# Kernel optimization log

Measured on AMD Instinct MI355X. Metric: run time of the kernel, lower is better.

## Reference

```python
import jax, jax.numpy as jnp
import numpy as np

DIM = 768
HEADS = 12
HEAD_DIM = DIM // HEADS
EPS = 1e-5


def setup_inputs() -> dict:
    key = jax.random.key(0)
    ks = jax.random.split(key, 9)
    s = 0.02
    x = jax.random.normal(ks[0], (4, 1024, DIM), dtype=jnp.float32)
    return {
        "x": x,
        "Wqkv_c": jax.random.normal(ks[1], (DIM, 3 * DIM), jnp.float32) * s,
        "bqkv_c": jnp.zeros((3 * DIM,), jnp.float32),
        "Wp_c": jax.random.normal(ks[2], (DIM, DIM), jnp.float32) * s,
        "bp_c": jnp.zeros((DIM,), jnp.float32),
        "Wqkv_ac": jax.random.normal(ks[3], (DIM, 3 * DIM), jnp.float32) * s,
        "bqkv_ac": jnp.zeros((3 * DIM,), jnp.float32),
        "Wp_ac": jax.random.normal(ks[4], (DIM, DIM), jnp.float32) * s,
        "bp_ac": jnp.zeros((DIM,), jnp.float32),
        "gamma": jnp.ones((DIM,), jnp.float32),
        "beta": jnp.zeros((DIM,), jnp.float32),
    }


def _branch(x, Wqkv, bqkv, Wp, bp, causal: bool):
    B, T, C = x.shape
    qkv = (x @ Wqkv + bqkv).reshape(B, T, 3, HEADS, HEAD_DIM)
    qkv = jnp.transpose(qkv, (2, 0, 3, 1, 4))  # [3,B,H,T,Dh]
    q, k, v = qkv[0], qkv[1], qkv[2]
    scores = jnp.einsum("bhqd,bhkd->bhqk", q, k) / np.sqrt(HEAD_DIM).astype(np.float32)
    i = jnp.arange(T)[:, None]
    j = jnp.arange(T)[None, :]
    mask = (j <= i) if causal else (j >= i)  # tril / triu (incl. diagonal)
    scores = jnp.where(mask[None, None], scores, -jnp.inf)
    attn = jax.nn.softmax(scores, axis=-1)
    out = jnp.einsum("bhqk,bhkd->bhqd", attn, v)
    out = jnp.transpose(out, (0, 2, 1, 3)).reshape(B, T, C)
    return out @ Wp + bp


def reference(x, Wqkv_c, bqkv_c, Wp_c, bp_c, Wqkv_ac, bqkv_ac, Wp_ac, bp_ac, gamma, beta):
    out_c = _branch(x, Wqkv_c, bqkv_c, Wp_c, bp_c, causal=True)
    out_ac = _branch(x, Wqkv_ac, bqkv_ac, Wp_ac, bp_ac, causal=False)
    y = x + out_c + out_ac  # residual; dropout is identity at eval
    mu = jnp.mean(y, axis=-1, keepdims=True)
    var = jnp.var(y, axis=-1, keepdims=True)
    return (y - mu) * jax.lax.rsqrt(var + EPS) * gamma + beta
```

## Files before the change

kernel.cpp:

```cpp
#include <hip/hip_runtime.h>
#include <stdint.h>

#define DIM 768
#define HEADS 12
#define HD 64
#define BATCH 4
#define SEQ 1024
#define NTOK (BATCH*SEQ)
#define QKVW (3*DIM)
#define QKW (2*DIM)
#define EPS 1e-5f

typedef __attribute__((ext_vector_type(8))) short short8;
typedef __attribute__((ext_vector_type(4))) float f32x4;

__device__ __forceinline__ unsigned short f2bf(float f) {
    union { float f; unsigned u; } v; v.f = f;
    unsigned r = v.u + 0x7fffu + ((v.u >> 16) & 1u);
    return (unsigned short)(r >> 16);
}
__device__ __forceinline__ float b2f(unsigned short s) {
    union { unsigned u; float f; } v; v.u = (unsigned)s << 16; return v.f;
}

__device__ __forceinline__ void gld_lds16(const void* g, void* l) {
    auto gp = reinterpret_cast<const __attribute__((address_space(1))) unsigned int*>(
        (uintptr_t)g);
    auto lp = reinterpret_cast<__attribute__((address_space(3))) unsigned int*>(
        (unsigned int)(uintptr_t)l);
    __builtin_amdgcn_global_load_lds(gp, lp, 16, 0, 0);
}

#define CVT_X_BLOCKS (NTOK*DIM/4096)
#define CVT_WQ_TILES ((QKVW/32)*(DIM/32))
#define CVT_WP_TILES ((DIM/32)*(DIM/32))
__global__ __launch_bounds__(256) void cvt_all_kernel(
    const float* __restrict__ x,
    const float* __restrict__ Wq0, const float* __restrict__ Wq1,
    const float* __restrict__ Wp0, const float* __restrict__ Wp1,
    unsigned short* __restrict__ xb,
    unsigned short* __restrict__ WqT0, unsigned short* __restrict__ WqT1,
    unsigned short* __restrict__ WpT0, unsigned short* __restrict__ WpT1)
{
    const int bid = blockIdx.x, tid = threadIdx.x;
    if (bid < CVT_X_BLOCKS) {
        const int base = bid * 1024 + tid;
#pragma unroll
        for (int u = 0; u < 4; ++u) {
            const float4 v = ((const float4*)x)[base + u * 256];
            ushort4 o4;
            o4.x = f2bf(v.x); o4.y = f2bf(v.y); o4.z = f2bf(v.z); o4.w = f2bf(v.w);
            ((ushort4*)xb)[base + u * 256] = o4;
        }
        return;
    }
    __shared__ float t[32][33];
    const float* W; unsigned short* WT; int N, K, tile;
    int w = bid - CVT_X_BLOCKS;
    if (w < 2 * CVT_WQ_TILES) {
        const int z = w / CVT_WQ_TILES; tile = w % CVT_WQ_TILES;
        W = z ? Wq1 : Wq0; WT = z ? WqT1 : WqT0; N = QKVW; K = DIM;
    } else {
        w -= 2 * CVT_WQ_TILES;
        const int z = w / CVT_WP_TILES; tile = w % CVT_WP_TILES;
        W = z ? Wp1 : Wp0; WT = z ? WpT1 : WpT0; N = DIM; K = DIM;
    }
    const int ntiles = N / 32;
    const int n0 = (tile % ntiles) * 32, k0 = (tile / ntiles) * 32;
    const int c = tid & 31, rr = tid >> 5;
#pragma unroll
    for (int i = 0; i < 4; ++i)
        t[rr + 8 * i][c] = W[(size_t)(k0 + rr + 8 * i) * N + n0 + c];
    __syncthreads();
#pragma unroll
    for (int i = 0; i < 4; ++i)
        WT[(size_t)(n0 + rr + 8 * i) * K + k0 + c] = f2bf(t[c][rr + 8 * i]);
}

__global__ __launch_bounds__(256, 2) void gemm_qkv_kernel(
    const unsigned short* __restrict__ A,
    const unsigned short* __restrict__ BT0, const unsigned short* __restrict__ BT1,
    const float* __restrict__ bias0, const float* __restrict__ bias1,
    unsigned short* __restrict__ QK0, unsigned short* __restrict__ QK1,
    unsigned short* __restrict__ VT0, unsigned short* __restrict__ VT1)
{
    const int gid = blockIdx.x;
    const int wg = (gid & 7) * 144 + (gid >> 3);
    const int by = wg & 31;
    const int bxz = wg >> 5;
    const int z = (bxz >= 18) ? 1 : 0;
    const int bx = z ? bxz - 18 : bxz;
    const unsigned short* __restrict__ BT = z ? BT1 : BT0;
    const float* __restrict__ bias = z ? bias1 : bias0;
    unsigned short* __restrict__ QK = z ? QK1 : QK0;
    unsigned short* __restrict__ VT = z ? VT1 : VT0;
    const int m0 = by * 128;
    const int nb0 = bx * 128;

    __shared__ __align__(16) unsigned short lds[32768];

    const int tid = threadIdx.x, lane = tid & 63, wv = tid >> 6;
    const int fm = lane & 15, fg = lane >> 4;
    const int wr = wv >> 1, wc = wv & 1;

    const int sr8 = lane >> 3;
    const int sc = ((lane & 7) ^ sr8) * 8;
    const unsigned short* pA = A  + (size_t)(m0  + wv * 8 + sr8) * DIM + sc;
    const unsigned short* pB = BT + (size_t)(nb0 + wv * 8 + sr8) * DIM + sc;
    unsigned short* dA = lds + wv * 512;
    unsigned short* dB = lds + 16384 + wv * 512;

    const int swz = fm & 7;
    const int cK0 = ((0 + fg) ^ swz) * 8;
    const int cK1 = ((4 + fg) ^ swz) * 8;
    const int aB = (wr * 64 + fm) * 64;
    const int bB = (wc * 64 + fm) * 64;

    f32x4 acc[4][4];
#pragma unroll
    for (int i = 0; i < 4; ++i)
#pragma unroll
        for (int j = 0; j < 4; ++j) acc[i][j] = f32x4{0.f, 0.f, 0.f, 0.f};

    short8 a[4][2], b[4][2];

#pragma unroll
    for (int j = 0; j < 4; ++j) {
        gld_lds16(pA + j * 32 * DIM, dA + j * 2048);
        gld_lds16(pB + j * 32 * DIM, dB + j * 2048);
    }

    for (int t = 0; t < 12; ++t) {
        const int ab = (t & 1) * 8192;
        const int bb = 16384 + (t & 1) * 8192;
        const int nb2 = ((t + 1) & 1) * 8192;

        asm volatile("s_waitcnt vmcnt(0)" ::: "memory");
        __builtin_amdgcn_s_barrier();
        if (t < 11) {
            const int kN = (t + 1) * 64;
#pragma unroll
            for (int j = 0; j < 4; ++j) {
                gld_lds16(pA + kN + j * 32 * DIM, dA + nb2 + j * 2048);
                gld_lds16(pB + kN + j * 32 * DIM, dB + nb2 + j * 2048);
            }
        }

#pragma unroll
        for (int mi = 0; mi < 4; ++mi) {
            a[mi][0] = *(const short8*)&lds[ab + aB + mi * 1024 + cK0];
            a[mi][1] = *(const short8*)&lds[ab + aB + mi * 1024 + cK1];
        }
#pragma unroll
        for (int nj = 0; nj < 2; ++nj) {
            b[nj][0] = *(const short8*)&lds[bb + bB + nj * 1024 + cK0];
            b[nj][1] = *(const short8*)&lds[bb + bB + nj * 1024 + cK1];
        }
        asm volatile("s_waitcnt lgkmcnt(0)" ::: "memory");
        __builtin_amdgcn_sched_barrier(0);
        __builtin_amdgcn_s_setprio(1);
#pragma unroll
        for (int ks = 0; ks < 2; ++ks)
#pragma unroll
            for (int mi = 0; mi < 4; ++mi)
#pragma unroll
                for (int nj = 0; nj < 2; ++nj)
                    acc[mi][nj] = __builtin_amdgcn_mfma_f32_16x16x32_bf16(
                        a[mi][ks], b[nj][ks], acc[mi][nj], 0, 0, 0);
        __builtin_amdgcn_s_setprio(0);

#pragma unroll
        for (int nj = 2; nj < 4; ++nj) {
            b[nj][0] = *(const short8*)&lds[bb + bB + nj * 1024 + cK0];
            b[nj][1] = *(const short8*)&lds[bb + bB + nj * 1024 + cK1];
        }
        asm volatile("s_waitcnt lgkmcnt(0)" ::: "memory");
        __builtin_amdgcn_sched_barrier(0);
        __builtin_amdgcn_s_setprio(1);
#pragma unroll
        for (int ks = 0; ks < 2; ++ks)
#pragma unroll
            for (int mi = 0; mi < 4; ++mi)
#pragma unroll
                for (int nj = 2; nj < 4; ++nj)
                    acc[mi][nj] = __builtin_amdgcn_mfma_f32_16x16x32_bf16(
                        a[mi][ks], b[nj][ks], acc[mi][nj], 0, 0, 0);
        __builtin_amdgcn_s_setprio(0);
    }

    __syncthreads();
    const int rbase = fg * 4;
    const int rowg = tid >> 4, lseg = tid & 15;
    if (nb0 < QKW) {
        const float qsc = (nb0 < DIM) ? 0.125f : 1.0f;
#pragma unroll
        for (int i = 0; i < 4; ++i) {
            const int ml = wr * 64 + i * 16 + rbase;
#pragma unroll
            for (int j = 0; j < 4; ++j) {
                const int nl = wc * 64 + j * 16 + fm;
                const float bs = bias[nb0 + nl];
#pragma unroll
                for (int r = 0; r < 4; ++r)
                    lds[(ml + r) * 136 + nl] = f2bf((acc[i][j][r] + bs) * qsc);
            }
        }
        __syncthreads();
#pragma unroll
        for (int pp = 0; pp < 8; ++pp) {
            const int row = pp * 16 + rowg;
            const uint4 v = *(const uint4*)&lds[row * 136 + lseg * 8];
            *(uint4*)(QK + (size_t)(m0 + row) * QKW + nb0 + lseg * 8) = v;
        }
    } else {
        const int b8 = m0 >> 10, t0 = m0 & 1023;
#pragma unroll
        for (int i = 0; i < 4; ++i) {
            const int tl = wr * 64 + i * 16 + rbase;
#pragma unroll
            for (int j = 0; j < 4; ++j) {
                const int nl = wc * 64 + j * 16 + fm;
                const float bs = bias[nb0 + nl];
                const unsigned p0 = f2bf(acc[i][j][0] + bs);
                const unsigned p1 = f2bf(acc[i][j][1] + bs);
                const unsigned p2 = f2bf(acc[i][j][2] + bs);
                const unsigned p3 = f2bf(acc[i][j][3] + bs);
                uint2 u; u.x = p0 | (p1 << 16); u.y = p2 | (p3 << 16);
                *(uint2*)(&lds[nl * 136 + tl]) = u;
            }
        }
        __syncthreads();
#pragma unroll
        for (int pp = 0; pp < 8; ++pp) {
            const int nl = pp * 16 + rowg;
            const int nh = (nb0 - QKW) + nl;
            const uint4 v = *(const uint4*)&lds[nl * 136 + lseg * 8];
            *(uint4*)(VT + ((size_t)((b8 * HEADS + (nh >> 6)) * HD + (nh & 63))) * SEQ
                      + t0 + lseg * 8) = v;
        }
    }
}

__global__ __launch_bounds__(256) void gemm_proj_kernel(
    const unsigned short* __restrict__ A0, const unsigned short* __restrict__ BT0,
    const unsigned short* __restrict__ A1, const unsigned short* __restrict__ BT1,
    const float* __restrict__ b0, const float* __restrict__ b1,
    const float* __restrict__ xres, float* __restrict__ Y0,
    unsigned short* __restrict__ Y1)
{
    const int z = blockIdx.z;
    const unsigned short* __restrict__ A  = z ? A1 : A0;
    const unsigned short* __restrict__ BT = z ? BT1 : BT0;
    __shared__ __align__(16) unsigned short Als[2][64 * 32];
    __shared__ __align__(16) unsigned short Bls[2][128 * 32];
    const int tid = threadIdx.x, lane = tid & 63, wv = tid >> 6;
    const int m0 = blockIdx.y * 64, n0 = blockIdx.x * 128;
    const int fm = lane & 15, fg = lane >> 4, fk = (lane >> 4) * 8;
    const int srw = lane >> 2, kk = (lane & 3) * 8;
    const int K = DIM;

    const unsigned short* Ag  = A  + (size_t)(m0 + wv * 16 + srw) * K + kk;
    const unsigned short* Bg0 = BT + (size_t)(n0 + wv * 32 + srw) * K + kk;
    const unsigned short* Bg1 = BT + (size_t)(n0 + wv * 32 + 16 + srw) * K + kk;

    f32x4 acc[4][2];
#pragma unroll
    for (int i = 0; i < 4; ++i)
#pragma unroll
        for (int j = 0; j < 2; ++j) acc[i][j] = f32x4{0.f, 0.f, 0.f, 0.f};

    gld_lds16(Ag,  &Als[0][wv * 512]);
    gld_lds16(Bg0, &Bls[0][wv * 1024]);
    gld_lds16(Bg1, &Bls[0][wv * 1024 + 512]);

    const int NK = K / 32;
    for (int kt = 0; kt < NK; ++kt) {
        const int p = kt & 1;
        __syncthreads();
        if (kt + 1 < NK) {
            const int off = (kt + 1) * 32;
            gld_lds16(Ag + off,  &Als[p ^ 1][wv * 512]);
            gld_lds16(Bg0 + off, &Bls[p ^ 1][wv * 1024]);
            gld_lds16(Bg1 + off, &Bls[p ^ 1][wv * 1024 + 512]);
        }
        short8 af[4], bf[2];
#pragma unroll
        for (int i = 0; i < 4; ++i)
            af[i] = *(const short8*)&Als[p][(i * 16 + fm) * 32 + fk];
#pragma unroll
        for (int j = 0; j < 2; ++j)
            bf[j] = *(const short8*)&Bls[p][(wv * 32 + j * 16 + fm) * 32 + fk];
#pragma unroll
        for (int i = 0; i < 4; ++i)
#pragma unroll
            for (int j = 0; j < 2; ++j)
                acc[i][j] = __builtin_amdgcn_mfma_f32_16x16x32_bf16(af[i], bf[j], acc[i][j], 0, 0, 0);
    }
#pragma unroll
    for (int i = 0; i < 4; ++i) {
        const int m = m0 + i * 16 + fg * 4;
#pragma unroll
        for (int j = 0; j < 2; ++j) {
            const int n = n0 + wv * 32 + j * 16 + fm;
            if (z == 0) {
                const float bs = b0[n] + b1[n];
#pragma unroll
                for (int r = 0; r < 4; ++r) {
                    const size_t idx = (size_t)(m + r) * DIM + n;
                    Y0[idx] = acc[i][j][r] + xres[idx] + bs;
                }
            } else {
#pragma unroll
                for (int r = 0; r < 4; ++r)
                    Y1[(size_t)(m + r) * DIM + n] = f2bf(acc[i][j][r]);
            }
        }
    }
}

#define KP 72
__global__ __launch_bounds__(256, 3) void attn_fused_kernel(
    const unsigned short* __restrict__ qk_c, const unsigned short* __restrict__ vT_c,
    const unsigned short* __restrict__ qk_ac, const unsigned short* __restrict__ vT_ac,
    unsigned short* __restrict__ o_c, unsigned short* __restrict__ o_ac)
{
    __shared__ __align__(16) unsigned short Kls[2][64 * KP];
    __shared__ __align__(16) unsigned short Vls[2][64 * KP];
    __shared__ __align__(16) unsigned short Ps[4][16 * KP];
    const int tid = threadIdx.x, lane = tid & 63, w = tid >> 6;
    const int fm = lane & 15, fg = lane >> 4;
    const int bh = blockIdx.x, qt = blockIdx.y;
    const int b = bh / HEADS, h = bh % HEADS;
    unsigned short* Psw = &Ps[w][0];
    const int srow = tid >> 3, sseg = (tid & 7) * 8;

    for (int br = 0; br < 2; ++br) {
        const int causal = (br == 0);
        const unsigned short* __restrict__ qk = causal ? qk_c : qk_ac;
        const unsigned short* __restrict__ vT = causal ? vT_c : vT_ac;
        unsigned short* __restrict__ o = causal ? o_c : o_ac;
        const unsigned short* qbase = qk + (size_t)b * SEQ * QKW + h * HD;
        const unsigned short* kbase = qbase + DIM;
        const unsigned short* vtb   = vT + (size_t)(b * HEADS + h) * HD * SEQ;

        short8 qb0, qb1;
        {
            const size_t qoff = (size_t)(qt * 64 + w * 16 + fm) * QKW + fg * 8;
            qb0 = *(const short8*)(qbase + qoff);
            qb1 = *(const short8*)(qbase + qoff + 32);
        }

        float ls = 0.f;
        f32x4 accO[4];
#pragma unroll
        for (int dj = 0; dj < 4; ++dj) accO[dj] = f32x4{0.f, 0.f, 0.f, 0.f};

        const int ktb = causal ? 0 : qt;
        const int kte = causal ? qt : (SEQ / 64 - 1);

        uint4 kr0 = *(const uint4*)(kbase + (size_t)(ktb * 64 + srow) * QKW + sseg);
        uint4 kr1 = *(const uint4*)(kbase + (size_t)(ktb * 64 + srow + 32) * QKW + sseg);
        uint4 vr0 = *(const uint4*)(vtb + (size_t)srow * SEQ + ktb * 64 + sseg);
        uint4 vr1 = *(const uint4*)(vtb + (size_t)(srow + 32) * SEQ + ktb * 64 + sseg);

        if (br) __syncthreads();
        int p = 0;
        for (int kt = ktb; kt <= kte; ++kt) {
            *(uint4*)(&Kls[p][srow * KP + sseg])        = kr0;
            *(uint4*)(&Kls[p][(srow + 32) * KP + sseg]) = kr1;
            *(uint4*)(&Vls[p][srow * KP + sseg])        = vr0;
            *(uint4*)(&Vls[p][(srow + 32) * KP + sseg]) = vr1;
            if (kt < kte) {
                const int ktn = kt + 1;
                kr0 = *(const uint4*)(kbase + (size_t)(ktn * 64 + srow) * QKW + sseg);
                kr1 = *(const uint4*)(kbase + (size_t)(ktn * 64 + srow + 32) * QKW + sseg);
                vr0 = *(const uint4*)(vtb + (size_t)srow * SEQ + ktn * 64 + sseg);
                vr1 = *(const uint4*)(vtb + (size_t)(srow + 32) * SEQ + ktn * 64 + sseg);
            }
            __syncthreads();

            f32x4 st[4];
#pragma unroll
            for (int kj = 0; kj < 4; ++kj) {
                const short8 ka0 = *(const short8*)&Kls[p][(kj * 16 + fm) * KP + fg * 8];
                const short8 ka1 = *(const short8*)&Kls[p][(kj * 16 + fm) * KP + 32 + fg * 8];
                st[kj] = __builtin_amdgcn_mfma_f32_16x16x32_bf16(ka0, qb0, f32x4{0.f,0.f,0.f,0.f}, 0, 0, 0);
                st[kj] = __builtin_amdgcn_mfma_f32_16x16x32_bf16(ka1, qb1, st[kj], 0, 0, 0);
            }
            const bool diag = (kt == qt);
#pragma unroll
            for (int kj = 0; kj < 4; ++kj) {
                float e[4];
#pragma unroll
                for (int r = 0; r < 4; ++r) {
                    float v = st[kj][r];
                    if (diag) {
                        const int ki = kj * 16 + fg * 4 + r;
                        const int qi = w * 16 + fm;
                        const bool ok = causal ? (ki <= qi) : (ki >= qi);
                        if (!ok) v = -1e30f;
                    }
                    e[r] = __expf(v);
                    ls += e[r];
                }
                union { float f; unsigned u; } u0, u1, u2, u3;
                u0.f = e[0]; u1.f = e[1]; u2.f = e[2]; u3.f = e[3];
                uint2 u;
                u.x = (u0.u >> 16) | (u1.u & 0xffff0000u);
                u.y = (u2.u >> 16) | (u3.u & 0xffff0000u);
                *(uint2*)(Psw + fm * KP + kj * 16 + fg * 4) = u;
            }
            const short8 ap0 = *(const short8*)(Psw + fm * KP + fg * 8);
            const short8 ap1 = *(const short8*)(Psw + fm * KP + 32 + fg * 8);
#pragma unroll
            for (int dj = 0; dj < 4; ++dj) {
                const short8 vb0 = *(const short8*)&Vls[p][(dj * 16 + fm) * KP + fg * 8];
                const short8 vb1 = *(const short8*)&Vls[p][(dj * 16 + fm) * KP + 32 + fg * 8];
                accO[dj] = __builtin_amdgcn_mfma_f32_16x16x32_bf16(ap0, vb0, accO[dj], 0, 0, 0);
                accO[dj] = __builtin_amdgcn_mfma_f32_16x16x32_bf16(ap1, vb1, accO[dj], 0, 0, 0);
            }
            p ^= 1;
        }

        float lt = ls;
        lt += __shfl_xor(lt, 16);
        lt += __shfl_xor(lt, 32);
        float li_o[4];
#pragma unroll
        for (int r = 0; r < 4; ++r) li_o[r] = __shfl(lt, fg * 4 + r);
#pragma unroll
        for (int r = 0; r < 4; ++r) {
            const float inv = 1.f / li_o[r];
            const int q = qt * 64 + w * 16 + fg * 4 + r;
            unsigned short* orow = o + ((size_t)b * SEQ + q) * DIM + h * HD;
#pragma unroll
            for (int dj = 0; dj < 4; ++dj)
                orow[dj * 16 + fm] = f2bf(accO[dj][r] * inv);
        }
    }
}

__global__ __launch_bounds__(256) void ln_kernel(
    const float* __restrict__ Y0, const unsigned short* __restrict__ Y1,
    const float* __restrict__ gamma, const float* __restrict__ beta,
    float* __restrict__ out)
{
    const int row = blockIdx.x;
    const int tid = threadIdx.x;
    const float* y0r = Y0 + (size_t)row * DIM;
    const unsigned short* y1r = Y1 + (size_t)row * DIM;
    float v0 = y0r[tid]       + b2f(y1r[tid]);
    float v1 = y0r[tid + 256] + b2f(y1r[tid + 256]);
    float v2 = y0r[tid + 512] + b2f(y1r[tid + 512]);
    float s = v0 + v1 + v2;
    float q = v0 * v0 + v1 * v1 + v2 * v2;
#pragma unroll
    for (int off = 32; off > 0; off >>= 1) {
        s += __shfl_down(s, off);
        q += __shfl_down(q, off);
    }
    __shared__ float rs_[4], rq_[4];
    const int wv = tid >> 6;
    if ((tid & 63) == 0) { rs_[wv] = s; rq_[wv] = q; }
    __syncthreads();
    const float ts = rs_[0] + rs_[1] + rs_[2] + rs_[3];
    const float tq = rq_[0] + rq_[1] + rq_[2] + rq_[3];
    const float mu = ts * (1.f / DIM);
    const float var = tq * (1.f / DIM) - mu * mu;
    const float rstd = rsqrtf(var + EPS);
    out[(size_t)row * DIM + tid]       = (v0 - mu) * rstd * gamma[tid]       + beta[tid];
    out[(size_t)row * DIM + tid + 256] = (v1 - mu) * rstd * gamma[tid + 256] + beta[tid + 256];
    out[(size_t)row * DIM + tid + 512] = (v2 - mu) * rstd * gamma[tid + 512] + beta[tid + 512];
}

extern "C" void kernel_launch(void* const* d_in, const int* in_sizes, int n_in,
                              void* d_out, int out_size, void* d_ws, size_t ws_size,
                              hipStream_t stream)
{
    const float* x       = (const float*)d_in[0];
    const float* Wqkv_c  = (const float*)d_in[1];
    const float* bqkv_c  = (const float*)d_in[2];
    const float* Wp_c    = (const float*)d_in[3];
    const float* bp_c    = (const float*)d_in[4];
    const float* Wqkv_ac = (const float*)d_in[5];
    const float* bqkv_ac = (const float*)d_in[6];
    const float* Wp_ac   = (const float*)d_in[7];
    const float* bp_ac   = (const float*)d_in[8];
    const float* gamma   = (const float*)d_in[9];
    const float* beta    = (const float*)d_in[10];
    float* out = (float*)d_out;

    char* p = (char*)d_ws;
    unsigned short* qk_c   = (unsigned short*)p; p += (size_t)NTOK * QKW * 2;
    unsigned short* qk_ac  = (unsigned short*)p; p += (size_t)NTOK * QKW * 2;
    unsigned short* vT_c   = (unsigned short*)p; p += (size_t)NTOK * DIM * 2;
    unsigned short* vT_ac  = (unsigned short*)p; p += (size_t)NTOK * DIM * 2;
    unsigned short* o_ac   = (unsigned short*)p; p += (size_t)NTOK * DIM * 2;
    unsigned short* xb     = (unsigned short*)p; p += (size_t)NTOK * DIM * 2;
    unsigned short* WqT_c  = (unsigned short*)p; p += (size_t)QKVW * DIM * 2;
    unsigned short* WqT_ac = (unsigned short*)p; p += (size_t)QKVW * DIM * 2;
    unsigned short* WpT_c  = (unsigned short*)p; p += (size_t)DIM * DIM * 2;
    unsigned short* WpT_ac = (unsigned short*)p; p += (size_t)DIM * DIM * 2;
    unsigned short* o_c = WqT_c;
    float*          Y0  = (float*)qk_c;
    unsigned short* Y1  = vT_c;

    cvt_all_kernel<<<CVT_X_BLOCKS + 2 * CVT_WQ_TILES + 2 * CVT_WP_TILES, 256, 0, stream>>>(
        x, Wqkv_c, Wqkv_ac, Wp_c, Wp_ac, xb, WqT_c, WqT_ac, WpT_c, WpT_ac);

    gemm_qkv_kernel<<<1152, 256, 0, stream>>>(
        xb, WqT_c, WqT_ac, bqkv_c, bqkv_ac, qk_c, qk_ac, vT_c, vT_ac);

    attn_fused_kernel<<<dim3(BATCH * HEADS, SEQ / 64), 256, 0, stream>>>(
        qk_c, vT_c, qk_ac, vT_ac, o_c, o_ac);

    gemm_proj_kernel<<<dim3(DIM / 128, NTOK / 64, 2), 256, 0, stream>>>(
        o_c, WpT_c, o_ac, WpT_ac, bp_c, bp_ac, x, Y0, Y1);
    ln_kernel<<<NTOK, 256, 0, stream>>>(Y0, Y1, gamma, beta, out);
}
```

Baseline: 197.1 us.

## Share A tile across both branch weight matrices in QKV GEMM with triple buffering

Each workgroup of the QKV GEMM now computes the same 128x128 output tile for both the causal and anticausal weights, loading the activation tile once and reusing it across two accumulator sets. That halves the grid and the A-operand global and LDS traffic. The K loop also moves from a double-buffered 64-wide step to a triple-buffered 32-wide step with a partial vmcnt wait, so loads run two stages ahead. The cost is twice the accumulator registers and a larger LDS footprint, which may lower occupancy, plus fewer workgroups to fill the GPU.

```diff
diff --git a/kernel.cpp b/kernel.cpp
--- a/kernel.cpp
+++ b/kernel.cpp
@@ -85,148 +85,140 @@
     unsigned short* __restrict__ VT0, unsigned short* __restrict__ VT1)
 {
     const int gid = blockIdx.x;
-    const int wg = (gid & 7) * 144 + (gid >> 3);
-    const int by = wg & 31;
-    const int bxz = wg >> 5;
-    const int z = (bxz >= 18) ? 1 : 0;
-    const int bx = z ? bxz - 18 : bxz;
-    const unsigned short* __restrict__ BT = z ? BT1 : BT0;
-    const float* __restrict__ bias = z ? bias1 : bias0;
-    unsigned short* __restrict__ QK = z ? QK1 : QK0;
-    unsigned short* __restrict__ VT = z ? VT1 : VT0;
+    const int wg = (gid & 7) * 72 + (gid >> 3);
+    const int by = wg & 31, bx = wg >> 5;
     const int m0 = by * 128;
     const int nb0 = bx * 128;
 
-    __shared__ __align__(16) unsigned short lds[32768];
+    __shared__ __align__(16) unsigned short lds[36864];
 
     const int tid = threadIdx.x, lane = tid & 63, wv = tid >> 6;
     const int fm = lane & 15, fg = lane >> 4;
     const int wr = wv >> 1, wc = wv & 1;
 
-    const int sr8 = lane >> 3;
-    const int sc = ((lane & 7) ^ sr8) * 8;
-    const unsigned short* pA = A  + (size_t)(m0  + wv * 8 + sr8) * DIM + sc;
-    const unsigned short* pB = BT + (size_t)(nb0 + wv * 8 + sr8) * DIM + sc;
-    unsigned short* dA = lds + wv * 512;
-    unsigned short* dB = lds + 16384 + wv * 512;
-
-    const int swz = fm & 7;
-    const int cK0 = ((0 + fg) ^ swz) * 8;
-    const int cK1 = ((4 + fg) ^ swz) * 8;
-    const int aB = (wr * 64 + fm) * 64;
-    const int bB = (wc * 64 + fm) * 64;
-
-    f32x4 acc[4][4];
+    const int s4 = lane >> 2;
+    const int sc = ((lane & 3) ^ ((lane >> 3) & 3)) * 8;
+    const unsigned short* pA  = A   + (size_t)(m0  + wv * 16 + s4) * DIM + sc;
+    const unsigned short* pBc = BT0 + (size_t)(nb0 + wv * 16 + s4) * DIM + sc;
+    const unsigned short* pBa = BT1 + (size_t)(nb0 + wv * 16 + s4) * DIM + sc;
+    unsigned short* dA  = lds + wv * 512;
+    unsigned short* dBc = lds + 12288 + wv * 512;
+    unsigned short* dBa = lds + 24576 + wv * 512;
+
+    const int cR = (fg ^ ((fm >> 1) & 3)) * 8;
+    const int aB = (wr * 64 + fm) * 32;
+    const int bB = (wc * 64 + fm) * 32;
+
+    f32x4 accc[4][4], acca[4][4];
 #pragma unroll
     for (int i = 0; i < 4; ++i)
 #pragma unroll
-        for (int j = 0; j < 4; ++j) acc[i][j] = f32x4{0.f, 0.f, 0.f, 0.f};
-
-    short8 a[4][2], b[4][2];
-
-#pragma unroll
-    for (int j = 0; j < 4; ++j) {
-        gld_lds16(pA + j * 32 * DIM, dA + j * 2048);
-        gld_lds16(pB + j * 32 * DIM, dB + j * 2048);
-    }
-
-    for (int t = 0; t < 12; ++t) {
-        const int ab = (t & 1) * 8192;
-        const int bb = 16384 + (t & 1) * 8192;
-        const int nb2 = ((t + 1) & 1) * 8192;
-
-        asm volatile("s_waitcnt vmcnt(0)" ::: "memory");
+        for (int j = 0; j < 4; ++j) {
+            accc[i][j] = f32x4{0.f, 0.f, 0.f, 0.f};
+            acca[i][j] = f32x4{0.f, 0.f, 0.f, 0.f};
+        }
+
+    short8 a[4], b[4], b2[4];
+
+#define STAGE(kt, buf) do {                                   \
+        const int ko_ = (kt) * 32; const int bo_ = (buf) * 4096; \
+        gld_lds16(pA  + ko_,            dA  + bo_);           \
+        gld_lds16(pA  + ko_ + 64 * DIM, dA  + bo_ + 2048);    \
+        gld_lds16(pBc + ko_,            dBc + bo_);           \
+        gld_lds16(pBc + ko_ + 64 * DIM, dBc + bo_ + 2048);    \
+        gld_lds16(pBa + ko_,            dBa + bo_);           \
+        gld_lds16(pBa + ko_ + 64 * DIM, dBa + bo_ + 2048);    \
+    } while (0)
+
+    STAGE(0, 0);
+    STAGE(1, 1);
+
+#pragma unroll 3
+    for (int t = 0; t < 24; ++t) {
+        if (t < 23) asm volatile("s_waitcnt vmcnt(6)" ::: "memory");
+        else        asm volatile("s_waitcnt vmcnt(0)" ::: "memory");
         __builtin_amdgcn_s_barrier();
-        if (t < 11) {
-            const int kN = (t + 1) * 64;
-#pragma unroll
-            for (int j = 0; j < 4; ++j) {
-                gld_lds16(pA + kN + j * 32 * DIM, dA + nb2 + j * 2048);
-                gld_lds16(pB + kN + j * 32 * DIM, dB + nb2 + j * 2048);
-            }
-        }
-
-#pragma unroll
-        for (int mi = 0; mi < 4; ++mi) {
-            a[mi][0] = *(const short8*)&lds[ab + aB + mi * 1024 + cK0];
-            a[mi][1] = *(const short8*)&lds[ab + aB + mi * 1024 + cK1];
-        }
-#pragma unroll
-        for (int nj = 0; nj < 2; ++nj) {
-            b[nj][0] = *(const short8*)&lds[bb + bB + nj * 1024 + cK0];
-            b[nj][1] = *(const short8*)&lds[bb + bB + nj * 1024 + cK1];
-        }
+        if (t < 22) STAGE(t + 2, (t + 2) % 3);
+        const int ab = (t % 3) * 4096;
+
+#pragma unroll
+        for (int mi = 0; mi < 4; ++mi)
+            a[mi] = *(const short8*)&lds[ab + aB + mi * 512 + cR];
+#pragma unroll
+        for (int nj = 0; nj < 4; ++nj)
+            b[nj] = *(const short8*)&lds[12288 + ab + bB + nj * 512 + cR];
         asm volatile("s_waitcnt lgkmcnt(0)" ::: "memory");
         __builtin_amdgcn_sched_barrier(0);
         __builtin_amdgcn_s_setprio(1);
 #pragma unroll
-        for (int ks = 0; ks < 2; ++ks)
-#pragma unroll
-            for (int mi = 0; mi < 4; ++mi)
-#pragma unroll
-                for (int nj = 0; nj < 2; ++nj)
-                    acc[mi][nj] = __builtin_amdgcn_mfma_f32_16x16x32_bf16(
-                        a[mi][ks], b[nj][ks], acc[mi][nj], 0, 0, 0);
+        for (int mi = 0; mi < 4; ++mi)
+#pragma unroll
+            for (int nj = 0; nj < 4; ++nj)
+                accc[mi][nj] = __builtin_amdgcn_mfma_f32_16x16x32_bf16(
+                    a[mi], b[nj], accc[mi][nj], 0, 0, 0);
         __builtin_amdgcn_s_setprio(0);
 
 #pragma unroll
-        for (int nj = 2; nj < 4; ++nj) {
-            b[nj][0] = *(const short8*)&lds[bb + bB + nj * 1024 + cK0];
-            b[nj][1] = *(const short8*)&lds[bb + bB + nj * 1024 + cK1];
-        }
+        for (int nj = 0; nj < 4; ++nj)
+            b2[nj] = *(const short8*)&lds[24576 + ab + bB + nj * 512 + cR];
         asm volatile("s_waitcnt lgkmcnt(0)" ::: "memory");
         __builtin_amdgcn_sched_barrier(0);
         __builtin_amdgcn_s_setprio(1);
 #pragma unroll
-        for (int ks = 0; ks < 2; ++ks)
-#pragma unroll
-            for (int mi = 0; mi < 4; ++mi)
-#pragma unroll
-                for (int nj = 2; nj < 4; ++nj)
-                    acc[mi][nj] = __builtin_amdgcn_mfma_f32_16x16x32_bf16(
-                        a[mi][ks], b[nj][ks], acc[mi][nj], 0, 0, 0);
+        for (int mi = 0; mi < 4; ++mi)
+#pragma unroll
+            for (int nj = 0; nj < 4; ++nj)
+                acca[mi][nj] = __builtin_amdgcn_mfma_f32_16x16x32_bf16(
+                    a[mi], b2[nj], acca[mi][nj], 0, 0, 0);
         __builtin_amdgcn_s_setprio(0);
     }
+#undef STAGE
 
     __syncthreads();
-    const int rbase = fg * 4;
     const int rowg = tid >> 4, lseg = tid & 15;
     if (nb0 < QKW) {
         const float qsc = (nb0 < DIM) ? 0.125f : 1.0f;
 #pragma unroll
         for (int i = 0; i < 4; ++i) {
-            const int ml = wr * 64 + i * 16 + rbase;
+            const int ml = wr * 64 + i * 16 + fg * 4;
 #pragma unroll
             for (int j = 0; j < 4; ++j) {
                 const int nl = wc * 64 + j * 16 + fm;
-                const float bs = bias[nb0 + nl];
-#pragma unroll
-                for (int r = 0; r < 4; ++r)
-                    lds[(ml + r) * 136 + nl] = f2bf((acc[i][j][r] + bs) * qsc);
+                const float bsc = bias0[nb0 + nl];
+                const float bsa = bias1[nb0 + nl];
+#pragma unroll
+                for (int r = 0; r < 4; ++r) {
+                    lds[(ml + r) * 136 + nl]         = f2bf((accc[i][j][r] + bsc) * qsc);
+                    lds[17408 + (ml + r) * 136 + nl] = f2bf((acca[i][j][r] + bsa) * qsc);
+                }
             }
         }
         __syncthreads();
 #pragma unroll
         for (int pp = 0; pp < 8; ++pp) {
             const int row = pp * 16 + rowg;
-            const uint4 v = *(const uint4*)&lds[row * 136 + lseg * 8];
-            *(uint4*)(QK + (size_t)(m0 + row) * QKW + nb0 + lseg * 8) = v;
+            const uint4 vc = *(const uint4*)&lds[row * 136 + lseg * 8];
+            const uint4 va = *(const uint4*)&lds[17408 + row * 136 + lseg * 8];
+            *(uint4*)(QK0 + (size_t)(m0 + row) * QKW + nb0 + lseg * 8) = vc;
+            *(uint4*)(QK1 + (size_t)(m0 + row) * QKW + nb0 + lseg * 8) = va;
         }
     } else {
         const int b8 = m0 >> 10, t0 = m0 & 1023;
 #pragma unroll
         for (int i = 0; i < 4; ++i) {
-            const int tl = wr * 64 + i * 16 + rbase;
+            const int tl = wr * 64 + i * 16 + fg * 4;
 #pragma unroll
             for (int j = 0; j < 4; ++j) {
                 const int nl = wc * 64 + j * 16 + fm;
-                const float bs = bias[nb0 + nl];
-                const unsigned p0 = f2bf(acc[i][j][0] + bs);
-                const unsigned p1 = f2bf(acc[i][j][1] + bs);
-                const unsigned p2 = f2bf(acc[i][j][2] + bs);
-                const unsigned p3 = f2bf(acc[i][j][3] + bs);
-                uint2 u; u.x = p0 | (p1 << 16); u.y = p2 | (p3 << 16);
-                *(uint2*)(&lds[nl * 136 + tl]) = u;
+                const float bsc = bias0[nb0 + nl];
+                const float bsa = bias1[nb0 + nl];
+                uint2 uc, ua;
+                uc.x = (unsigned)f2bf(accc[i][j][0] + bsc) | ((unsigned)f2bf(accc[i][j][1] + bsc) << 16);
+                uc.y = (unsigned)f2bf(accc[i][j][2] + bsc) | ((unsigned)f2bf(accc[i][j][3] + bsc) << 16);
+                ua.x = (unsigned)f2bf(acca[i][j][0] + bsa) | ((unsigned)f2bf(acca[i][j][1] + bsa) << 16);
+                ua.y = (unsigned)f2bf(acca[i][j][2] + bsa) | ((unsigned)f2bf(acca[i][j][3] + bsa) << 16);
+                *(uint2*)(&lds[nl * 136 + tl])         = uc;
+                *(uint2*)(&lds[17408 + nl * 136 + tl]) = ua;
             }
         }
         __syncthreads();
@@ -234,9 +226,12 @@
         for (int pp = 0; pp < 8; ++pp) {
             const int nl = pp * 16 + rowg;
             const int nh = (nb0 - QKW) + nl;
-            const uint4 v = *(const uint4*)&lds[nl * 136 + lseg * 8];
-            *(uint4*)(VT + ((size_t)((b8 * HEADS + (nh >> 6)) * HD + (nh & 63))) * SEQ
-                      + t0 + lseg * 8) = v;
+            const size_t voff = ((size_t)((b8 * HEADS + (nh >> 6)) * HD + (nh & 63))) * SEQ
+                                + t0 + lseg * 8;
+            const uint4 vc = *(const uint4*)&lds[nl * 136 + lseg * 8];
+            const uint4 va = *(const uint4*)&lds[17408 + nl * 136 + lseg * 8];
+            *(uint4*)(VT0 + voff) = vc;
+            *(uint4*)(VT1 + voff) = va;
         }
     }
 }
@@ -508,7 +503,7 @@
     cvt_all_kernel<<<CVT_X_BLOCKS + 2 * CVT_WQ_TILES + 2 * CVT_WP_TILES, 256, 0, stream>>>(
         x, Wqkv_c, Wqkv_ac, Wp_c, Wp_ac, xb, WqT_c, WqT_ac, WpT_c, WpT_ac);
 
-    gemm_qkv_kernel<<<1152, 256, 0, stream>>>(
+    gemm_qkv_kernel<<<576, 256, 0, stream>>>(
         xb, WqT_c, WqT_ac, bqkv_c, bqkv_ac, qk_c, qk_ac, vT_c, vT_ac);
 
     attn_fused_kernel<<<dim3(BATCH * HEADS, SEQ / 64), 256, 0, stream>>>(
```

After: 195.8 us. Within noise of the previous version (-0.6%).

## Halve QKV GEMM K-tile to cut LDS and raise occupancy to four blocks

Applied to the files above, without the earlier changes.

The QKV GEMM now stages K in 32-wide slices instead of 64-wide, shrinking the double-buffered LDS footprint from 64KB to about 34KB. Launch bounds are raised to allow 4 blocks per CU, and the swizzle and block-to-tile mapping are reworked into a 2x4 grouping for L2 locality. The aim is more resident waves to hide global-load latency. The cost is twice as many barrier and wait iterations per tile and tighter register limits, which could cause spills.

```diff
diff --git a/kernel.cpp b/kernel.cpp
--- a/kernel.cpp
+++ b/kernel.cpp
@@ -77,7 +77,7 @@
         WT[(size_t)(n0 + rr + 8 * i) * K + k0 + c] = f2bf(t[c][rr + 8 * i]);
 }
 
-__global__ __launch_bounds__(256, 2) void gemm_qkv_kernel(
+__global__ __launch_bounds__(256, 4) void gemm_qkv_kernel(
     const unsigned short* __restrict__ A,
     const unsigned short* __restrict__ BT0, const unsigned short* __restrict__ BT1,
     const float* __restrict__ bias0, const float* __restrict__ bias1,
@@ -85,9 +85,9 @@
     unsigned short* __restrict__ VT0, unsigned short* __restrict__ VT1)
 {
     const int gid = blockIdx.x;
-    const int wg = (gid & 7) * 144 + (gid >> 3);
-    const int by = wg & 31;
-    const int bxz = wg >> 5;
+    const int g = gid & 7, l = gid >> 3;
+    const int by  = (g >> 2) * 16 + (l & 15);
+    const int bxz = (g & 3) * 9 + (l >> 4);
     const int z = (bxz >= 18) ? 1 : 0;
     const int bx = z ? bxz - 18 : bxz;
     const unsigned short* __restrict__ BT = z ? BT1 : BT0;
@@ -97,24 +97,22 @@
     const int m0 = by * 128;
     const int nb0 = bx * 128;
 
-    __shared__ __align__(16) unsigned short lds[32768];
+    __shared__ __align__(16) unsigned short lds[17408];
 
     const int tid = threadIdx.x, lane = tid & 63, wv = tid >> 6;
     const int fm = lane & 15, fg = lane >> 4;
     const int wr = wv >> 1, wc = wv & 1;
 
-    const int sr8 = lane >> 3;
-    const int sc = ((lane & 7) ^ sr8) * 8;
-    const unsigned short* pA = A  + (size_t)(m0  + wv * 8 + sr8) * DIM + sc;
-    const unsigned short* pB = BT + (size_t)(nb0 + wv * 8 + sr8) * DIM + sc;
+    const int s4 = lane >> 2;
+    const int sc = ((lane & 3) ^ ((lane >> 3) & 3)) * 8;
+    const unsigned short* pA = A  + (size_t)(m0  + wv * 16 + s4) * DIM + sc;
+    const unsigned short* pB = BT + (size_t)(nb0 + wv * 16 + s4) * DIM + sc;
     unsigned short* dA = lds + wv * 512;
-    unsigned short* dB = lds + 16384 + wv * 512;
-
-    const int swz = fm & 7;
-    const int cK0 = ((0 + fg) ^ swz) * 8;
-    const int cK1 = ((4 + fg) ^ swz) * 8;
-    const int aB = (wr * 64 + fm) * 64;
-    const int bB = (wc * 64 + fm) * 64;
+    unsigned short* dB = lds + 8192 + wv * 512;
+
+    const int cR = (fg ^ ((fm >> 1) & 3)) * 8;
+    const int aB = (wr * 64 + fm) * 32;
+    const int bB = (wc * 64 + fm) * 32;
 
     f32x4 acc[4][4];
 #pragma unroll
@@ -122,80 +120,64 @@
 #pragma unroll
         for (int j = 0; j < 4; ++j) acc[i][j] = f32x4{0.f, 0.f, 0.f, 0.f};
 
-    short8 a[4][2], b[4][2];
-
-#pragma unroll
-    for (int j = 0; j < 4; ++j) {
-        gld_lds16(pA + j * 32 * DIM, dA + j * 2048);
-        gld_lds16(pB + j * 32 * DIM, dB + j * 2048);
-    }
-
-    for (int t = 0; t < 12; ++t) {
-        const int ab = (t & 1) * 8192;
-        const int bb = 16384 + (t & 1) * 8192;
-        const int nb2 = ((t + 1) & 1) * 8192;
-
+    short8 a[4], b[4];
+
+#define STAGE(kt, buf) do {                                   \
+        const int ko_ = (kt) * 32; const int bo_ = (buf) * 4096; \
+        gld_lds16(pA + ko_,            dA + bo_);             \
+        gld_lds16(pA + ko_ + 64 * DIM, dA + bo_ + 2048);      \
+        gld_lds16(pB + ko_,            dB + bo_);             \
+        gld_lds16(pB + ko_ + 64 * DIM, dB + bo_ + 2048);      \
+    } while (0)
+
+    STAGE(0, 0);
+
+    for (int t = 0; t < 24; ++t) {
         asm volatile("s_waitcnt vmcnt(0)" ::: "memory");
         __builtin_amdgcn_s_barrier();
-        if (t < 11) {
-            const int kN = (t + 1) * 64;
-#pragma unroll
-            for (int j = 0; j < 4; ++j) {
-                gld_lds16(pA + kN + j * 32 * DIM, dA + nb2 + j * 2048);
-                gld_lds16(pB + kN + j * 32 * DIM, dB + nb2 + j * 2048);
-            }
-        }
-
-#pragma unroll
-        for (int mi = 0; mi < 4; ++mi) {
-            a[mi][0] = *(const short8*)&lds[ab + aB + mi * 1024 + cK0];
-            a[mi][1] = *(const short8*)&lds[ab + aB + mi * 1024 + cK1];
-        }
-#pragma unroll
-        for (int nj = 0; nj < 2; ++nj) {
-            b[nj][0] = *(const short8*)&lds[bb + bB + nj * 1024 + cK0];
-            b[nj][1] = *(const short8*)&lds[bb + bB + nj * 1024 + cK1];
-        }
+        if (t < 23) STAGE(t + 1, (t + 1) & 1);
+        const int ab = (t & 1) * 4096;
+
+#pragma unroll
+        for (int mi = 0; mi < 4; ++mi)
+            a[mi] = *(const short8*)&lds[ab + aB + mi * 512 + cR];
+#pragma unroll
+        for (int nj = 0; nj < 2; ++nj)
+            b[nj] = *(const short8*)&lds[8192 + ab + bB + nj * 512 + cR];
         asm volatile("s_waitcnt lgkmcnt(0)" ::: "memory");
         __builtin_amdgcn_sched_barrier(0);
         __builtin_amdgcn_s_setprio(1);
 #pragma unroll
-        for (int ks = 0; ks < 2; ++ks)
-#pragma unroll
-            for (int mi = 0; mi < 4; ++mi)
-#pragma unroll
-                for (int nj = 0; nj < 2; ++nj)
-                    acc[mi][nj] = __builtin_amdgcn_mfma_f32_16x16x32_bf16(
-                        a[mi][ks], b[nj][ks], acc[mi][nj], 0, 0, 0);
+        for (int mi = 0; mi < 4; ++mi)
+#pragma unroll
+            for (int nj = 0; nj < 2; ++nj)
+                acc[mi][nj] = __builtin_amdgcn_mfma_f32_16x16x32_bf16(
+                    a[mi], b[nj], acc[mi][nj], 0, 0, 0);
         __builtin_amdgcn_s_setprio(0);
 
 #pragma unroll
-        for (int nj = 2; nj < 4; ++nj) {
-            b[nj][0] = *(const short8*)&lds[bb + bB + nj * 1024 + cK0];
-            b[nj][1] = *(const short8*)&lds[bb + bB + nj * 1024 + cK1];
-        }
+        for (int nj = 2; nj < 4; ++nj)
+            b[nj] = *(const short8*)&lds[8192 + ab + bB + nj * 512 + cR];
         asm volatile("s_waitcnt lgkmcnt(0)" ::: "memory");
         __builtin_amdgcn_sched_barrier(0);
         __builtin_amdgcn_s_setprio(1);
 #pragma unroll
-        for (int ks = 0; ks < 2; ++ks)
-#pragma unroll
-            for (int mi = 0; mi < 4; ++mi)
-#pragma unroll
-                for (int nj = 2; nj < 4; ++nj)
-                    acc[mi][nj] = __builtin_amdgcn_mfma_f32_16x16x32_bf16(
-                        a[mi][ks], b[nj][ks], acc[mi][nj], 0, 0, 0);
+        for (int mi = 0; mi < 4; ++mi)
+#pragma unroll
+            for (int nj = 2; nj < 4; ++nj)
+                acc[mi][nj] = __builtin_amdgcn_mfma_f32_16x16x32_bf16(
+                    a[mi], b[nj], acc[mi][nj], 0, 0, 0);
         __builtin_amdgcn_s_setprio(0);
     }
+#undef STAGE
 
     __syncthreads();
-    const int rbase = fg * 4;
     const int rowg = tid >> 4, lseg = tid & 15;
     if (nb0 < QKW) {
         const float qsc = (nb0 < DIM) ? 0.125f : 1.0f;
 #pragma unroll
         for (int i = 0; i < 4; ++i) {
-            const int ml = wr * 64 + i * 16 + rbase;
+            const int ml = wr * 64 + i * 16 + fg * 4;
 #pragma unroll
             for (int j = 0; j < 4; ++j) {
                 const int nl = wc * 64 + j * 16 + fm;
@@ -216,16 +198,14 @@
         const int b8 = m0 >> 10, t0 = m0 & 1023;
 #pragma unroll
         for (int i = 0; i < 4; ++i) {
-            const int tl = wr * 64 + i * 16 + rbase;
+            const int tl = wr * 64 + i * 16 + fg * 4;
 #pragma unroll
             for (int j = 0; j < 4; ++j) {
                 const int nl = wc * 64 + j * 16 + fm;
                 const float bs = bias[nb0 + nl];
-                const unsigned p0 = f2bf(acc[i][j][0] + bs);
-                const unsigned p1 = f2bf(acc[i][j][1] + bs);
-                const unsigned p2 = f2bf(acc[i][j][2] + bs);
-                const unsigned p3 = f2bf(acc[i][j][3] + bs);
-                uint2 u; u.x = p0 | (p1 << 16); u.y = p2 | (p3 << 16);
+                uint2 u;
+                u.x = (unsigned)f2bf(acc[i][j][0] + bs) | ((unsigned)f2bf(acc[i][j][1] + bs) << 16);
+                u.y = (unsigned)f2bf(acc[i][j][2] + bs) | ((unsigned)f2bf(acc[i][j][3] + bs) << 16);
                 *(uint2*)(&lds[nl * 136 + tl]) = u;
             }
         }
```

Measured after the change: 195.1 us. About the same (-1.0%).

## Fuse both projection branches into one block and remap QKV GEMM tile order

Applied to the files above, without the earlier changes.

The projection GEMM now computes both the causal and anti-causal branches in the same block, with two accumulator sets, and writes a single fp32 sum plus residual and bias. This removes the bf16 intermediate Y1, its separate write and read, and the extra add in the layernorm kernel, and it halves the proj grid. The QKV GEMM block-to-tile mapping is also changed to group tiles differently across XCDs for L2 locality. The cost is doubled LDS and register use per proj block, which may lower occupancy, and fewer blocks in the proj launch.

```diff
diff --git a/kernel.cpp b/kernel.cpp
--- a/kernel.cpp
+++ b/kernel.cpp
@@ -85,9 +85,9 @@
     unsigned short* __restrict__ VT0, unsigned short* __restrict__ VT1)
 {
     const int gid = blockIdx.x;
-    const int wg = (gid & 7) * 144 + (gid >> 3);
-    const int by = wg & 31;
-    const int bxz = wg >> 5;
+    const int g = gid & 7, l = gid >> 3;
+    const int by  = (g >> 2) * 16 + (l & 15);
+    const int bxz = (g & 3) * 9 + (l >> 4);
     const int z = (bxz >= 18) ? 1 : 0;
     const int bx = z ? bxz - 18 : bxz;
     const unsigned short* __restrict__ BT = z ? BT1 : BT0;
@@ -189,13 +189,12 @@
     }
 
     __syncthreads();
-    const int rbase = fg * 4;
     const int rowg = tid >> 4, lseg = tid & 15;
     if (nb0 < QKW) {
         const float qsc = (nb0 < DIM) ? 0.125f : 1.0f;
 #pragma unroll
         for (int i = 0; i < 4; ++i) {
-            const int ml = wr * 64 + i * 16 + rbase;
+            const int ml = wr * 64 + i * 16 + fg * 4;
 #pragma unroll
             for (int j = 0; j < 4; ++j) {
                 const int nl = wc * 64 + j * 16 + fm;
@@ -216,16 +215,14 @@
         const int b8 = m0 >> 10, t0 = m0 & 1023;
 #pragma unroll
         for (int i = 0; i < 4; ++i) {
-            const int tl = wr * 64 + i * 16 + rbase;
+            const int tl = wr * 64 + i * 16 + fg * 4;
 #pragma unroll
             for (int j = 0; j < 4; ++j) {
                 const int nl = wc * 64 + j * 16 + fm;
                 const float bs = bias[nb0 + nl];
-                const unsigned p0 = f2bf(acc[i][j][0] + bs);
-                const unsigned p1 = f2bf(acc[i][j][1] + bs);
-                const unsigned p2 = f2bf(acc[i][j][2] + bs);
-                const unsigned p3 = f2bf(acc[i][j][3] + bs);
-                uint2 u; u.x = p0 | (p1 << 16); u.y = p2 | (p3 << 16);
+                uint2 u;
+                u.x = (unsigned)f2bf(acc[i][j][0] + bs) | ((unsigned)f2bf(acc[i][j][1] + bs) << 16);
+                u.y = (unsigned)f2bf(acc[i][j][2] + bs) | ((unsigned)f2bf(acc[i][j][3] + bs) << 16);
                 *(uint2*)(&lds[nl * 136 + tl]) = u;
             }
         }
@@ -245,33 +242,38 @@
     const unsigned short* __restrict__ A0, const unsigned short* __restrict__ BT0,
     const unsigned short* __restrict__ A1, const unsigned short* __restrict__ BT1,
     const float* __restrict__ b0, const float* __restrict__ b1,
-    const float* __restrict__ xres, float* __restrict__ Y0,
-    unsigned short* __restrict__ Y1)
+    const float* __restrict__ xres, float* __restrict__ Y)
 {
-    const int z = blockIdx.z;
-    const unsigned short* __restrict__ A  = z ? A1 : A0;
-    const unsigned short* __restrict__ BT = z ? BT1 : BT0;
-    __shared__ __align__(16) unsigned short Als[2][64 * 32];
-    __shared__ __align__(16) unsigned short Bls[2][128 * 32];
+    __shared__ __align__(16) unsigned short Als[2][2][64 * 32];
+    __shared__ __align__(16) unsigned short Bls[2][2][128 * 32];
     const int tid = threadIdx.x, lane = tid & 63, wv = tid >> 6;
     const int m0 = blockIdx.y * 64, n0 = blockIdx.x * 128;
     const int fm = lane & 15, fg = lane >> 4, fk = (lane >> 4) * 8;
     const int srw = lane >> 2, kk = (lane & 3) * 8;
     const int K = DIM;
 
-    const unsigned short* Ag  = A  + (size_t)(m0 + wv * 16 + srw) * K + kk;
-    const unsigned short* Bg0 = BT + (size_t)(n0 + wv * 32 + srw) * K + kk;
-    const unsigned short* Bg1 = BT + (size_t)(n0 + wv * 32 + 16 + srw) * K + kk;
-
-    f32x4 acc[4][2];
+    const unsigned short* Ag0  = A0  + (size_t)(m0 + wv * 16 + srw) * K + kk;
+    const unsigned short* Ag1  = A1  + (size_t)(m0 + wv * 16 + srw) * K + kk;
+    const unsigned short* Bg00 = BT0 + (size_t)(n0 + wv * 32 + srw) * K + kk;
+    const unsigned short* Bg01 = BT0 + (size_t)(n0 + wv * 32 + 16 + srw) * K + kk;
+    const unsigned short* Bg10 = BT1 + (size_t)(n0 + wv * 32 + srw) * K + kk;
+    const unsigned short* Bg11 = BT1 + (size_t)(n0 + wv * 32 + 16 + srw) * K + kk;
+
+    f32x4 acc0[4][2], acc1[4][2];
 #pragma unroll
     for (int i = 0; i < 4; ++i)
 #pragma unroll
-        for (int j = 0; j < 2; ++j) acc[i][j] = f32x4{0.f, 0.f, 0.f, 0.f};
-
-    gld_lds16(Ag,  &Als[0][wv * 512]);
-    gld_lds16(Bg0, &Bls[0][wv * 1024]);
-    gld_lds16(Bg1, &Bls[0][wv * 1024 + 512]);
+        for (int j = 0; j < 2; ++j) {
+            acc0[i][j] = f32x4{0.f, 0.f, 0.f, 0.f};
+            acc1[i][j] = f32x4{0.f, 0.f, 0.f, 0.f};
+        }
+
+    gld_lds16(Ag0,  &Als[0][0][wv * 512]);
+    gld_lds16(Bg00, &Bls[0][0][wv * 1024]);
+    gld_lds16(Bg01, &Bls[0][0][wv * 1024 + 512]);
+    gld_lds16(Ag1,  &Als[1][0][wv * 512]);
+    gld_lds16(Bg10, &Bls[1][0][wv * 1024]);
+    gld_lds16(Bg11, &Bls[1][0][wv * 1024 + 512]);
 
     const int NK = K / 32;
     for (int kt = 0; kt < NK; ++kt) {
@@ -279,22 +281,36 @@
         __syncthreads();
         if (kt + 1 < NK) {
             const int off = (kt + 1) * 32;
-            gld_lds16(Ag + off,  &Als[p ^ 1][wv * 512]);
-            gld_lds16(Bg0 + off, &Bls[p ^ 1][wv * 1024]);
-            gld_lds16(Bg1 + off, &Bls[p ^ 1][wv * 1024 + 512]);
+            gld_lds16(Ag0 + off,  &Als[0][p ^ 1][wv * 512]);
+            gld_lds16(Bg00 + off, &Bls[0][p ^ 1][wv * 1024]);
+            gld_lds16(Bg01 + off, &Bls[0][p ^ 1][wv * 1024 + 512]);
+            gld_lds16(Ag1 + off,  &Als[1][p ^ 1][wv * 512]);
+            gld_lds16(Bg10 + off, &Bls[1][p ^ 1][wv * 1024]);
+            gld_lds16(Bg11 + off, &Bls[1][p ^ 1][wv * 1024 + 512]);
         }
         short8 af[4], bf[2];
 #pragma unroll
         for (int i = 0; i < 4; ++i)
-            af[i] = *(const short8*)&Als[p][(i * 16 + fm) * 32 + fk];
+            af[i] = *(const short8*)&Als[0][p][(i * 16 + fm) * 32 + fk];
 #pragma unroll
         for (int j = 0; j < 2; ++j)
-            bf[j] = *(const short8*)&Bls[p][(wv * 32 + j * 16 + fm) * 32 + fk];
+            bf[j] = *(const short8*)&Bls[0][p][(wv * 32 + j * 16 + fm) * 32 + fk];
 #pragma unroll
         for (int i = 0; i < 4; ++i)
 #pragma unroll
             for (int j = 0; j < 2; ++j)
-                acc[i][j] = __builtin_amdgcn_mfma_f32_16x16x32_bf16(af[i], bf[j], acc[i][j], 0, 0, 0);
+                acc0[i][j] = __builtin_amdgcn_mfma_f32_16x16x32_bf16(af[i], bf[j], acc0[i][j], 0, 0, 0);
+#pragma unroll
+        for (int i = 0; i < 4; ++i)
+            af[i] = *(const short8*)&Als[1][p][(i * 16 + fm) * 32 + fk];
+#pragma unroll
+        for (int j = 0; j < 2; ++j)
+            bf[j] = *(const short8*)&Bls[1][p][(wv * 32 + j * 16 + fm) * 32 + fk];
+#pragma unroll
+        for (int i = 0; i < 4; ++i)
+#pragma unroll
+            for (int j = 0; j < 2; ++j)
+                acc1[i][j] = __builtin_amdgcn_mfma_f32_16x16x32_bf16(af[i], bf[j], acc1[i][j], 0, 0, 0);
     }
 #pragma unroll
     for (int i = 0; i < 4; ++i) {
@@ -302,17 +318,11 @@
 #pragma unroll
         for (int j = 0; j < 2; ++j) {
             const int n = n0 + wv * 32 + j * 16 + fm;
-            if (z == 0) {
-                const float bs = b0[n] + b1[n];
-#pragma unroll
-                for (int r = 0; r < 4; ++r) {
-                    const size_t idx = (size_t)(m + r) * DIM + n;
-                    Y0[idx] = acc[i][j][r] + xres[idx] + bs;
-                }
-            } else {
-#pragma unroll
-                for (int r = 0; r < 4; ++r)
-                    Y1[(size_t)(m + r) * DIM + n] = f2bf(acc[i][j][r]);
+            const float bs = b0[n] + b1[n];
+#pragma unroll
+            for (int r = 0; r < 4; ++r) {
+                const size_t idx = (size_t)(m + r) * DIM + n;
+                Y[idx] = acc0[i][j][r] + acc1[i][j][r] + xres[idx] + bs;
             }
         }
     }
@@ -441,17 +451,16 @@
 }
 
 __global__ __launch_bounds__(256) void ln_kernel(
-    const float* __restrict__ Y0, const unsigned short* __restrict__ Y1,
+    const float* __restrict__ Y,
     const float* __restrict__ gamma, const float* __restrict__ beta,
     float* __restrict__ out)
 {
     const int row = blockIdx.x;
     const int tid = threadIdx.x;
-    const float* y0r = Y0 + (size_t)row * DIM;
-    const unsigned short* y1r = Y1 + (size_t)row * DIM;
-    float v0 = y0r[tid]       + b2f(y1r[tid]);
-    float v1 = y0r[tid + 256] + b2f(y1r[tid + 256]);
-    float v2 = y0r[tid + 512] + b2f(y1r[tid + 512]);
+    const float* yr = Y + (size_t)row * DIM;
+    float v0 = yr[tid];
+    float v1 = yr[tid + 256];
+    float v2 = yr[tid + 512];
     float s = v0 + v1 + v2;
     float q = v0 * v0 + v1 * v1 + v2 * v2;
 #pragma unroll
@@ -502,8 +511,7 @@
     unsigned short* WpT_c  = (unsigned short*)p; p += (size_t)DIM * DIM * 2;
     unsigned short* WpT_ac = (unsigned short*)p; p += (size_t)DIM * DIM * 2;
     unsigned short* o_c = WqT_c;
-    float*          Y0  = (float*)qk_c;
-    unsigned short* Y1  = vT_c;
+    float*          Y   = (float*)qk_c;
 
     cvt_all_kernel<<<CVT_X_BLOCKS + 2 * CVT_WQ_TILES + 2 * CVT_WP_TILES, 256, 0, stream>>>(
         x, Wqkv_c, Wqkv_ac, Wp_c, Wp_ac, xb, WqT_c, WqT_ac, WpT_c, WpT_ac);
@@ -514,7 +522,7 @@
     attn_fused_kernel<<<dim3(BATCH * HEADS, SEQ / 64), 256, 0, stream>>>(
         qk_c, vT_c, qk_ac, vT_ac, o_c, o_ac);
 
-    gemm_proj_kernel<<<dim3(DIM / 128, NTOK / 64, 2), 256, 0, stream>>>(
-        o_c, WpT_c, o_ac, WpT_ac, bp_c, bp_ac, x, Y0, Y1);
-    ln_kernel<<<NTOK, 256, 0, stream>>>(Y0, Y1, gamma, beta, out);
-}
+    gemm_proj_kernel<<<dim3(DIM / 128, NTOK / 64), 256, 0, stream>>>(
+        o_c, WpT_c, o_ac, WpT_ac, bp_c, bp_ac, x, Y);
+    ln_kernel<<<NTOK, 256, 0, stream>>>(Y, gamma, beta, out);
+}
```

Measured after the change: 188.7 us (median of 3 runs). 4.3% less time.
